# Performance work log

Hardware: AMD Instinct MI355X
Metric: run time of the kernel (lower is better)

The kernel has to match this reference:

```python
import jax, jax.numpy as jnp
from jax import lax
import numpy as np

N, C, H, W = 16, 256, 56, 56
K = 7          # unfold kernel positions along height
DIL = 3        # unfold dilation along height
PAD = 9        # unfold padding along height
DN = ('NCHW', 'OIHW', 'NCHW')


def setup_inputs() -> dict:
    key = jax.random.key(0)
    k0, k1, k2, k3 = jax.random.split(key, 4)
    x = jax.random.normal(k0, (N, C, H, W), dtype=jnp.float32)
    w1 = jax.random.normal(k1, (C, 1, 5, 5), dtype=jnp.float32) * 0.1   # depthwise 5x5
    w2 = jax.random.normal(k2, (C, 1, 3, 1), dtype=jnp.float32) * 0.2   # depthwise (3,1)
    w4 = jax.random.normal(k3, (C, C * K), dtype=jnp.float32) * (1.0 / np.sqrt(C * K))  # 1x1 mix
    return {"x": x, "w1": w1, "w2": w2, "w4": w4}


def reference(x, w1, w2, w4):
    n, c, h, w = x.shape
    # t_1: depthwise 5x5, padding 2
    t1 = lax.conv_general_dilated(x, w1, (1, 1), [(2, 2), (2, 2)],
                                  dimension_numbers=DN, feature_group_count=c)
    # t_2: depthwise (3,1), padding (1,0)
    t2 = lax.conv_general_dilated(x, w2, (1, 1), [(1, 1), (0, 0)],
                                  dimension_numbers=DN, feature_group_count=c)
    # F.unfold((7,1), dilation=(3,1), padding=(9,0)) -> (n, c, 7, h, w)
    t2p = jnp.pad(t2, ((0, 0), (0, 0), (PAD, PAD), (0, 0)))
    t3 = jnp.stack([t2p[:, :, DIL * k: DIL * k + h, :] for k in range(K)], axis=2)
    # 1x1 conv mixing c*7 -> c channels
    t4 = jnp.einsum('oi,nihw->nohw', w4, t3.reshape(n, c * K, h, w))
    # elementwise gate
    return t1 * t4
```

## Files before the change

kernel.cpp:

```cpp
#include <hip/hip_runtime.h>
#include <hip/hip_bf16.h>
#include <stdint.h>
#include <stddef.h>

#define AS1 __attribute__((address_space(1)))
#define AS3 __attribute__((address_space(3)))

typedef __attribute__((ext_vector_type(8))) __bf16 bf16x8;
typedef __attribute__((ext_vector_type(4))) float f32x4;
typedef __attribute__((ext_vector_type(4))) unsigned int u32x4;

static __device__ __forceinline__ unsigned short f2bf(float f) {
    unsigned u = __builtin_bit_cast(unsigned, f);
    u += 0x7FFFu + ((u >> 16) & 1u);
    return (unsigned short)(u >> 16);
}

__global__ __launch_bounds__(256) void k_t2prep(const float* __restrict__ x,
                                                const float* __restrict__ w2,
                                                unsigned short* __restrict__ t2p) {
    const int b = blockIdx.x;
    const int cc = (b & 7) * 32;
    const int g  = (b >> 3) % 19;
    const int n  = b / (19 * 8);
    const int t  = threadIdx.x;
    const int hp0 = g * 4;

    __shared__ float xs[6][32][57];
    const int hbase = hp0 - 10;
    const bool anyValid = (hp0 + 3 >= 9) && (hp0 <= 64);

    if (anyValid) {
        for (int idx = t; idx < 2688; idx += 256) {
            int r = idx / 448, rem = idx % 448;
            int ci = rem / 14, q = rem % 14;
            int hy = hbase + r;
            f32x4 v = {0.f, 0.f, 0.f, 0.f};
            if (hy >= 0 && hy < 56)
                v = *(const f32x4*)(x + ((size_t)(n * 256 + cc + ci) * 56 + hy) * 56 + q * 4);
            xs[r][ci][q * 4 + 0] = v[0];
            xs[r][ci][q * 4 + 1] = v[1];
            xs[r][ci][q * 4 + 2] = v[2];
            xs[r][ci][q * 4 + 3] = v[3];
        }
    }

    const int c = t & 31;
    const float a0 = w2[(cc + c) * 3 + 0];
    const float a1 = w2[(cc + c) * 3 + 1];
    const float a2 = w2[(cc + c) * 3 + 2];
    __syncthreads();

    #pragma unroll
    for (int j = 0; j < 4; ++j) {
        int hp = hp0 + j;
        if (hp >= 74) break;
        unsigned short* orow = t2p + (size_t)(n * 74 + hp) * (56 * 256);
        int h = hp - 9;
        if (h < 0 || h >= 56) {
            if (t < 224) {
                int w = t >> 2, c8 = (t & 3) * 8;
                u32x4 z = {0u, 0u, 0u, 0u};
                *(u32x4*)(orow + (size_t)w * 256 + cc + c8) = z;
            }
        } else {
            #pragma unroll
            for (int i = 0; i < 7; ++i) {
                int w = (t >> 5) + i * 8;
                float v = a0 * xs[j][c][w] + a1 * xs[j + 1][c][w] + a2 * xs[j + 2][c][w];
                orow[(size_t)w * 256 + cc + c] = f2bf(v);
            }
        }
    }
}

__global__ void k_w4conv(const float* __restrict__ w4, unsigned short* __restrict__ w4b) {
    int tid = blockIdx.x * 256 + threadIdx.x;
    int o = tid / 1792, j = tid % 1792;
    int k = j >> 8, c = j & 255;
    w4b[tid] = f2bf(w4[o * 1792 + c * 7 + k]);
}

__global__ __launch_bounds__(512, 2) void k_gemm8(const unsigned short* __restrict__ w4b,
                                                  const unsigned short* __restrict__ t2p,
                                                  float* __restrict__ out) {
    extern __shared__ char lds[];
    const int pix0 = blockIdx.x * 224;
    const int t = threadIdx.x;
    const int l = t & 63, wv = t >> 6;
    const int wr = wv >> 2, wc = wv & 3;
    const bool doB4 = (wv < 4);

    const char* w4c = (const char*)w4b;
    const char* t2c = (const char*)t2p;
    unsigned abase[4];
    {
        const int srow = t >> 3;
        const int segp = (t & 7) ^ (srow & 7);
        #pragma unroll
        for (int j = 0; j < 4; ++j)
            abase[j] = (unsigned)(j * 64 + srow) * 3584u + (unsigned)segp * 16u;
    }
    unsigned bbase[4];
    #pragma unroll
    for (int o = 0; o < 4; ++o) {
        int s = (o < 3) ? (t + (o << 9)) : (1536 + (t & 255));
        int row = s >> 3;
        int segp = (s & 7) ^ (row & 7);
        int P = pix0 + row;
        int n = P / 3136, rr = P % 3136;
        int hh = rr / 56, ww = rr % 56;
        bbase[o] = (unsigned)(((n * 74 + hh) * 56 + ww) * 512) + (unsigned)segp * 16u;
    }

#define STAGE(kk_, boff_) do {                                                        \
    unsigned _ao = (unsigned)(kk_) * 128u;                                            \
    unsigned _bo = (unsigned)((kk_) >> 2) * 86016u + (unsigned)((kk_) & 3) * 128u;    \
    _Pragma("unroll")                                                                 \
    for (int _j = 0; _j < 4; ++_j)                                                    \
        __builtin_amdgcn_global_load_lds((const AS1 void*)(w4c + abase[_j] + _ao),    \
            (AS3 void*)(lds + (boff_) + _j * 8192 + wv * 1024), 16, 0, 0);            \
    _Pragma("unroll")                                                                 \
    for (int _o = 0; _o < 3; ++_o)                                                    \
        __builtin_amdgcn_global_load_lds((const AS1 void*)(t2c + bbase[_o] + _bo),    \
            (AS3 void*)(lds + (boff_) + 32768 + _o * 8192 + wv * 1024), 16, 0, 0);    \
    if (doB4)                                                                         \
        __builtin_amdgcn_global_load_lds((const AS1 void*)(t2c + bbase[3] + _bo),     \
            (AS3 void*)(lds + (boff_) + 32768 + 24576 + wv * 1024), 16, 0, 0);        \
} while (0)

    const int lr = l & 15, lg = l >> 4;
    const int sx = lr & 7;
    const unsigned fo0 = (unsigned)((lg ^ sx) << 4);
    const unsigned fo1 = (unsigned)(((lg + 4) ^ sx) << 4);
    const unsigned aRow = (unsigned)(wc * 8192 + lr * 128);
    const unsigned bRow = (unsigned)(32768 + wr * 14336 + lr * 128);

    f32x4 acc[7][4];
    #pragma unroll
    for (int m = 0; m < 7; ++m)
        #pragma unroll
        for (int nn = 0; nn < 4; ++nn)
            acc[m][nn] = (f32x4){0.f, 0.f, 0.f, 0.f};

    bf16x8 afrag[4][2];

#define BCHUNK(M0_, CUR_) do {                                                         \
    bf16x8 _b00 = *(const bf16x8*)(lds + (CUR_) + bRow + (M0_) * 2048 + fo0);          \
    bf16x8 _b01 = *(const bf16x8*)(lds + (CUR_) + bRow + (M0_) * 2048 + fo1);          \
    bf16x8 _b10 = *(const bf16x8*)(lds + (CUR_) + bRow + ((M0_) + 1) * 2048 + fo0);    \
    bf16x8 _b11 = *(const bf16x8*)(lds + (CUR_) + bRow + ((M0_) + 1) * 2048 + fo1);    \
    __builtin_amdgcn_s_setprio(1);                                                     \
    _Pragma("unroll")                                                                  \
    for (int _n = 0; _n < 4; ++_n) {                                                   \
        acc[(M0_)][_n]     = __builtin_amdgcn_mfma_f32_16x16x32_bf16(afrag[_n][0], _b00, acc[(M0_)][_n], 0, 0, 0);     \
        acc[(M0_)][_n]     = __builtin_amdgcn_mfma_f32_16x16x32_bf16(afrag[_n][1], _b01, acc[(M0_)][_n], 0, 0, 0);     \
        acc[(M0_) + 1][_n] = __builtin_amdgcn_mfma_f32_16x16x32_bf16(afrag[_n][0], _b10, acc[(M0_) + 1][_n], 0, 0, 0); \
        acc[(M0_) + 1][_n] = __builtin_amdgcn_mfma_f32_16x16x32_bf16(afrag[_n][1], _b11, acc[(M0_) + 1][_n], 0, 0, 0); \
    }                                                                                  \
    __builtin_amdgcn_s_setprio(0);                                                     \
} while (0)

    STAGE(0, 0);

    for (int kk = 0; kk < 28; ++kk) {
        const unsigned cur = (kk & 1) ? 61440u : 0u;
        const unsigned nxt = cur ^ 61440u;
        const int kst = (kk < 27) ? kk + 1 : 27;

        STAGE(kst, nxt);
        if (doB4) { asm volatile("s_waitcnt vmcnt(8)" ::: "memory"); }
        else      { asm volatile("s_waitcnt vmcnt(7)" ::: "memory"); }
        __builtin_amdgcn_s_barrier();
        asm volatile("" ::: "memory");

        #pragma unroll
        for (int nn = 0; nn < 4; ++nn) {
            afrag[nn][0] = *(const bf16x8*)(lds + cur + aRow + nn * 2048 + fo0);
            afrag[nn][1] = *(const bf16x8*)(lds + cur + aRow + nn * 2048 + fo1);
        }
        BCHUNK(0, cur);
        BCHUNK(2, cur);
        BCHUNK(4, cur);
        {
            bf16x8 _b60 = *(const bf16x8*)(lds + cur + bRow + 6 * 2048 + fo0);
            bf16x8 _b61 = *(const bf16x8*)(lds + cur + bRow + 6 * 2048 + fo1);
            __builtin_amdgcn_s_setprio(1);
            #pragma unroll
            for (int _n = 0; _n < 4; ++_n) {
                acc[6][_n] = __builtin_amdgcn_mfma_f32_16x16x32_bf16(afrag[_n][0], _b60, acc[6][_n], 0, 0, 0);
                acc[6][_n] = __builtin_amdgcn_mfma_f32_16x16x32_bf16(afrag[_n][1], _b61, acc[6][_n], 0, 0, 0);
            }
            __builtin_amdgcn_s_setprio(0);
        }

        __builtin_amdgcn_s_barrier();
        asm volatile("" ::: "memory");
    }
#undef BCHUNK
#undef STAGE

    #pragma unroll
    for (int m = 0; m < 7; ++m) {
        int P = pix0 + wr * 112 + m * 16 + lr;
        int n = P / 3136, p = P % 3136;
        float* ob = out + (size_t)n * 802816 + p;
        #pragma unroll
        for (int nn = 0; nn < 4; ++nn) {
            int o = wc * 64 + nn * 16 + lg * 4;
            float* op = ob + (size_t)o * 3136;
            op[0 * 3136] = acc[m][nn][0];
            op[1 * 3136] = acc[m][nn][1];
            op[2 * 3136] = acc[m][nn][2];
            op[3 * 3136] = acc[m][nn][3];
        }
    }
}

__global__ __launch_bounds__(256) void k_gate(const float* __restrict__ x,
                                              const float* __restrict__ w1,
                                              float* __restrict__ out) {
    const int b = blockIdx.x;
    const int c = b & 255, n = b >> 8;
    const int t = threadIdx.x;
    __shared__ float xs[60][60];

    float* lp = &xs[0][0];
    #pragma unroll
    for (int i = 0; i < 15; ++i) {
        int idx = t + i * 256;
        if (idx < 3600) lp[idx] = 0.f;
    }
    __syncthreads();

    const float* xc = x + (size_t)(n * 256 + c) * 3136;
    #pragma unroll
    for (int k = 0; k < 4; ++k) {
        int j = t + k * 256;
        if (j < 784) {
            f32x4 v = *(const f32x4*)(xc + j * 4);
            int p = j * 4;
            int h = p / 56, w = p % 56;
            xs[h + 2][w + 2 + 0] = v[0];
            xs[h + 2][w + 2 + 1] = v[1];
            xs[h + 2][w + 2 + 2] = v[2];
            xs[h + 2][w + 2 + 3] = v[3];
        }
    }

    const float* wk = w1 + c * 25;
    float wr[25];
    #pragma unroll
    for (int i = 0; i < 25; ++i) wr[i] = wk[i];
    __syncthreads();

    float* oc = out + (size_t)(n * 256 + c) * 3136;
    #pragma unroll
    for (int k = 0; k < 4; ++k) {
        int j = t + k * 256;
        if (j < 784) {
            int p = j * 4;
            int h = p / 56, w = p % 56;
            f32x4 o = *(f32x4*)(oc + p);
            f32x4 t1 = {0.f, 0.f, 0.f, 0.f};
            #pragma unroll
            for (int dy = 0; dy < 5; ++dy)
                #pragma unroll
                for (int dx = 0; dx < 5; ++dx) {
                    float wv = wr[dy * 5 + dx];
                    t1[0] = fmaf(wv, xs[h + dy][w + dx + 0], t1[0]);
                    t1[1] = fmaf(wv, xs[h + dy][w + dx + 1], t1[1]);
                    t1[2] = fmaf(wv, xs[h + dy][w + dx + 2], t1[2]);
                    t1[3] = fmaf(wv, xs[h + dy][w + dx + 3], t1[3]);
                }
            o *= t1;
            *(f32x4*)(oc + p) = o;
        }
    }
}

extern "C" void kernel_launch(void* const* d_in, const int* in_sizes, int n_in,
                              void* d_out, int out_size, void* d_ws, size_t ws_size,
                              hipStream_t stream) {
    const float* x  = (const float*)d_in[0];
    const float* w1 = (const float*)d_in[1];
    const float* w2 = (const float*)d_in[2];
    const float* w4 = (const float*)d_in[3];
    float* out = (float*)d_out;

    const size_t W4B_ELEMS = 256 * 1792;
    const size_t T2P_ELEMS = (size_t)16 * 74 * 56 * 256;
    if (ws_size < (W4B_ELEMS + T2P_ELEMS) * sizeof(unsigned short)) return;
    unsigned short* w4b = (unsigned short*)d_ws;
    unsigned short* t2p = w4b + W4B_ELEMS;

    k_w4conv<<<1792, 256, 0, stream>>>(w4, w4b);
    k_t2prep<<<16 * 8 * 19, 256, 0, stream>>>(x, w2, t2p);
    k_gemm8<<<224, 512, 122880, stream>>>(w4b, t2p, out);
    k_gate<<<4096, 256, 0, stream>>>(x, w1, out);
}
```

Before: 116.6 us.

## Retile GEMM to 128x128 blocks with 256 threads over a 2D grid

The GEMM moves from 224-pixel by all-256-output tiles with 512 threads to 128x128 tiles with 256 threads on a 392x2 grid. Each wave now computes a 64x64 sub-tile and LDS per block drops to 64 KB. This gives 784 blocks instead of 224 so the 256 CUs are better filled, and it removes the uneven B-load path. The cost is that A and B are each reused less per block, which raises global and L2 traffic.

```diff
diff --git a/kernel.cpp b/kernel.cpp
--- a/kernel.cpp
+++ b/kernel.cpp
@@ -81,37 +81,30 @@
     w4b[tid] = f2bf(w4[o * 1792 + c * 7 + k]);
 }
 
-__global__ __launch_bounds__(512, 2) void k_gemm8(const unsigned short* __restrict__ w4b,
-                                                  const unsigned short* __restrict__ t2p,
-                                                  float* __restrict__ out) {
+__global__ __launch_bounds__(256, 2) void k_gemm(const unsigned short* __restrict__ w4b,
+                                                 const unsigned short* __restrict__ t2p,
+                                                 float* __restrict__ out) {
     extern __shared__ char lds[];
-    const int pix0 = blockIdx.x * 224;
+    const int pix0 = blockIdx.x * 128;
+    const int o0   = blockIdx.y * 128;
     const int t = threadIdx.x;
     const int l = t & 63, wv = t >> 6;
-    const int wr = wv >> 2, wc = wv & 3;
-    const bool doB4 = (wv < 4);
-
+    const int lr = l & 15, lg = l >> 4;
+
+    const int srow = t >> 3;
+    const int segp = (t & 7) ^ (srow & 7);
+    unsigned abase[4], bbase[4];
+    #pragma unroll
+    for (int j = 0; j < 4; ++j) {
+        int arow = j * 32 + srow;
+        abase[j] = (unsigned)(o0 + arow) * 3584u + (unsigned)segp * 16u;
+        int P = pix0 + j * 32 + srow;
+        int n = P / 3136, r = P % 3136;
+        int hh = r / 56, ww = r % 56;
+        bbase[j] = (unsigned)(((n * 74 + hh) * 56 + ww) * 512) + (unsigned)segp * 16u;
+    }
     const char* w4c = (const char*)w4b;
     const char* t2c = (const char*)t2p;
-    unsigned abase[4];
-    {
-        const int srow = t >> 3;
-        const int segp = (t & 7) ^ (srow & 7);
-        #pragma unroll
-        for (int j = 0; j < 4; ++j)
-            abase[j] = (unsigned)(j * 64 + srow) * 3584u + (unsigned)segp * 16u;
-    }
-    unsigned bbase[4];
-    #pragma unroll
-    for (int o = 0; o < 4; ++o) {
-        int s = (o < 3) ? (t + (o << 9)) : (1536 + (t & 255));
-        int row = s >> 3;
-        int segp = (s & 7) ^ (row & 7);
-        int P = pix0 + row;
-        int n = P / 3136, rr = P % 3136;
-        int hh = rr / 56, ww = rr % 56;
-        bbase[o] = (unsigned)(((n * 74 + hh) * 56 + ww) * 512) + (unsigned)segp * 16u;
-    }
 
 #define STAGE(kk_, boff_) do {                                                        \
     unsigned _ao = (unsigned)(kk_) * 128u;                                            \
@@ -119,26 +112,22 @@
     _Pragma("unroll")                                                                 \
     for (int _j = 0; _j < 4; ++_j)                                                    \
         __builtin_amdgcn_global_load_lds((const AS1 void*)(w4c + abase[_j] + _ao),    \
-            (AS3 void*)(lds + (boff_) + _j * 8192 + wv * 1024), 16, 0, 0);            \
+            (AS3 void*)(lds + (boff_) + _j * 4096 + wv * 1024), 16, 0, 0);            \
     _Pragma("unroll")                                                                 \
-    for (int _o = 0; _o < 3; ++_o)                                                    \
-        __builtin_amdgcn_global_load_lds((const AS1 void*)(t2c + bbase[_o] + _bo),    \
-            (AS3 void*)(lds + (boff_) + 32768 + _o * 8192 + wv * 1024), 16, 0, 0);    \
-    if (doB4)                                                                         \
-        __builtin_amdgcn_global_load_lds((const AS1 void*)(t2c + bbase[3] + _bo),     \
-            (AS3 void*)(lds + (boff_) + 32768 + 24576 + wv * 1024), 16, 0, 0);        \
+    for (int _j = 0; _j < 4; ++_j)                                                    \
+        __builtin_amdgcn_global_load_lds((const AS1 void*)(t2c + bbase[_j] + _bo),    \
+            (AS3 void*)(lds + (boff_) + 16384 + _j * 4096 + wv * 1024), 16, 0, 0);    \
 } while (0)
 
-    const int lr = l & 15, lg = l >> 4;
     const int sx = lr & 7;
     const unsigned fo0 = (unsigned)((lg ^ sx) << 4);
     const unsigned fo1 = (unsigned)(((lg + 4) ^ sx) << 4);
-    const unsigned aRow = (unsigned)(wc * 8192 + lr * 128);
-    const unsigned bRow = (unsigned)(32768 + wr * 14336 + lr * 128);
-
-    f32x4 acc[7][4];
-    #pragma unroll
-    for (int m = 0; m < 7; ++m)
+    const unsigned aRow = (unsigned)(((wv & 1) * 64 + lr) * 128);
+    const unsigned bRow = (unsigned)(16384 + ((wv >> 1) * 64 + lr) * 128);
+
+    f32x4 acc[4][4];
+    #pragma unroll
+    for (int m = 0; m < 4; ++m)
         #pragma unroll
         for (int nn = 0; nn < 4; ++nn)
             acc[m][nn] = (f32x4){0.f, 0.f, 0.f, 0.f};
@@ -164,13 +153,12 @@
     STAGE(0, 0);
 
     for (int kk = 0; kk < 28; ++kk) {
-        const unsigned cur = (kk & 1) ? 61440u : 0u;
-        const unsigned nxt = cur ^ 61440u;
+        const unsigned cur = (kk & 1) ? 32768u : 0u;
+        const unsigned nxt = cur ^ 32768u;
         const int kst = (kk < 27) ? kk + 1 : 27;
 
         STAGE(kst, nxt);
-        if (doB4) { asm volatile("s_waitcnt vmcnt(8)" ::: "memory"); }
-        else      { asm volatile("s_waitcnt vmcnt(7)" ::: "memory"); }
+        asm volatile("s_waitcnt vmcnt(8)" ::: "memory");
         __builtin_amdgcn_s_barrier();
         asm volatile("" ::: "memory");
 
@@ -181,18 +169,6 @@
         }
         BCHUNK(0, cur);
         BCHUNK(2, cur);
-        BCHUNK(4, cur);
-        {
-            bf16x8 _b60 = *(const bf16x8*)(lds + cur + bRow + 6 * 2048 + fo0);
-            bf16x8 _b61 = *(const bf16x8*)(lds + cur + bRow + 6 * 2048 + fo1);
-            __builtin_amdgcn_s_setprio(1);
-            #pragma unroll
-            for (int _n = 0; _n < 4; ++_n) {
-                acc[6][_n] = __builtin_amdgcn_mfma_f32_16x16x32_bf16(afrag[_n][0], _b60, acc[6][_n], 0, 0, 0);
-                acc[6][_n] = __builtin_amdgcn_mfma_f32_16x16x32_bf16(afrag[_n][1], _b61, acc[6][_n], 0, 0, 0);
-            }
-            __builtin_amdgcn_s_setprio(0);
-        }
 
         __builtin_amdgcn_s_barrier();
         asm volatile("" ::: "memory");
@@ -201,13 +177,13 @@
 #undef STAGE
 
     #pragma unroll
-    for (int m = 0; m < 7; ++m) {
-        int P = pix0 + wr * 112 + m * 16 + lr;
+    for (int m = 0; m < 4; ++m) {
+        int P = pix0 + (wv >> 1) * 64 + m * 16 + lr;
         int n = P / 3136, p = P % 3136;
         float* ob = out + (size_t)n * 802816 + p;
         #pragma unroll
         for (int nn = 0; nn < 4; ++nn) {
-            int o = wc * 64 + nn * 16 + lg * 4;
+            int o = o0 + (wv & 1) * 64 + nn * 16 + lg * 4;
             float* op = ob + (size_t)o * 3136;
             op[0 * 3136] = acc[m][nn][0];
             op[1 * 3136] = acc[m][nn][1];
@@ -296,6 +272,6 @@
 
     k_w4conv<<<1792, 256, 0, stream>>>(w4, w4b);
     k_t2prep<<<16 * 8 * 19, 256, 0, stream>>>(x, w2, t2p);
-    k_gemm8<<<224, 512, 122880, stream>>>(w4b, t2p, out);
+    k_gemm<<<dim3(392, 2), 256, 65536, stream>>>(w4b, t2p, out);
     k_gate<<<4096, 256, 0, stream>>>(x, w1, out);
 }
```

Measured after the change: 126.0 us. +8.0%, slower.
